# Kernel tuning notes

Measured on AMD Instinct MI355X. Metric: run time of the kernel, lower is better.

The kernel has to match this reference:

```python
import jax, jax.numpy as jnp
import numpy as np

N = 50000      # nodes
E = 800000     # top-down edges (before self-loops)
IN = 256       # in_dim
HID = 64       # hidden_dim
H = 4          # heads
SLOPE = 0.2    # PyG GATConv leaky_relu negative_slope


def setup_inputs() -> dict:
    key = jax.random.key(0)
    ks = jax.random.split(key, 12)
    g = lambda k, s, fan: jax.random.normal(k, s, dtype=jnp.float32) / np.float32(np.sqrt(fan))
    return {
        "x": jax.random.normal(ks[0], (N, IN), dtype=jnp.float32),
        "root_features": jax.random.normal(ks[1], (N, IN), dtype=jnp.float32),
        "edge_index": jax.random.randint(ks[2], (2, E), 0, N, dtype=jnp.int32),
        "W1": g(ks[3], (H * HID, IN), IN),
        "a_src1": g(ks[4], (H, HID), HID),
        "a_dst1": g(ks[5], (H, HID), HID),
        "b1": jnp.zeros((H * HID,), jnp.float32),
        "W2": g(ks[6], (H * HID, H * HID), H * HID),
        "a_src2": g(ks[7], (H, HID), HID),
        "a_dst2": g(ks[8], (H, HID), HID),
        "b2": jnp.zeros((HID,), jnp.float32),
        "Wr": g(ks[9], (HID, IN), IN),
        "br": jnp.zeros((HID,), jnp.float32),
    }


def gat_conv(h_in, src, dst, W, a_src, a_dst, bias, concat):
    """PyG GATConv (eval mode): gather -> attention logit -> segment softmax -> scatter."""
    h = (h_in @ W.T).reshape(-1, H, HID)                 # [N, H, C]
    alpha_s = jnp.einsum('nhc,hc->nh', h, a_src)         # [N, H]
    alpha_d = jnp.einsum('nhc,hc->nh', h, a_dst)
    logits = jax.nn.leaky_relu(alpha_s[src] + alpha_d[dst], SLOPE)   # [Etot, H]
    # numerically stable softmax over incoming edges of each dst node
    m = jax.ops.segment_max(logits, dst, num_segments=N)             # [N, H]
    e = jnp.exp(logits - m[dst])
    denom = jax.ops.segment_sum(e, dst, num_segments=N)              # [N, H]
    alpha = e / denom[dst]                                           # self-loops => denom > 0
    out = jax.ops.segment_sum(alpha[:, :, None] * h[src], dst, num_segments=N)  # [N, H, C]
    if concat:
        return out.reshape(-1, H * HID) + bias
    return out.mean(axis=1) + bias


def reference(x, root_features, edge_index, W1, a_src1, a_dst1, b1,
              W2, a_src2, a_dst2, b2, Wr, br):
    # PyG GATConv adds self-loops by default
    loops = jnp.arange(N, dtype=edge_index.dtype)
    src = jnp.concatenate([edge_index[0], loops])   # parents (message sources)
    dst = jnp.concatenate([edge_index[1], loops])   # children (aggregation targets)

    h = gat_conv(x, src, dst, W1, a_src1, a_dst1, b1, concat=True)   # [N, H*HID]
    h = jax.nn.relu(h)                                               # dropout = identity in eval
    h = gat_conv(h, src, dst, W2, a_src2, a_dst2, b2, concat=False)  # [N, HID]
    return h + root_features @ Wr.T + br
```

## Files before the change

kernel.cpp:

```cpp
#include <hip/hip_runtime.h>
#include <hip/hip_bf16.h>
#include <math.h>

#define NN   50000
#define EE   800000
#define ETOT (EE + NN)
#define KDIM 256
#define HEADS 4
#define HIDD 64
#define DCAP 64

typedef float  f32x4  __attribute__((ext_vector_type(4)));
typedef short  bf16x8 __attribute__((ext_vector_type(8)));

__device__ __forceinline__ float b2f(unsigned short u) {
    union { float f; unsigned int i; } v; v.i = (unsigned int)u << 16; return v.f;
}
__device__ __forceinline__ unsigned short f2b(float f) {
    union { float f; unsigned int i; } v; v.f = f;
    return (unsigned short)((v.i + 0x7fffu + ((v.i >> 16) & 1u)) >> 16);
}
__device__ __forceinline__ float lrelu(float x) { return x >= 0.f ? x : 0.2f * x; }

#define CASTB 144

__global__ __launch_bounds__(256) void prep_k(
    const float* __restrict__ W1, const float* __restrict__ W2,
    const float* __restrict__ Wr, unsigned short* __restrict__ wout)
{
    int i = (blockIdx.x * 256 + threadIdx.x) * 4;
    const float* src;
    int off;
    if (i < 65536)        { src = W1; off = 0; }
    else if (i < 131072)  { src = W2; off = 65536; }
    else                  { src = Wr; off = 131072; }
    float4 v = *reinterpret_cast<const float4*>(src + (i - off));
    ushort4 o;
    o.x = f2b(v.x); o.y = f2b(v.y); o.z = f2b(v.z); o.w = f2b(v.w);
    *reinterpret_cast<ushort4*>(wout + i) = o;
}

template<bool AF32, int NCT, bool ALPHA, bool OUTF32>
__device__ __forceinline__ void gemm_body(
    unsigned short* __restrict__ WlRaw, int bid,
    const void* __restrict__ Ain, const unsigned short* __restrict__ W,
    void* __restrict__ Cout, int Mrows,
    const float* __restrict__ av_src, const float* __restrict__ av_dst,
    float* __restrict__ AS, float* __restrict__ AD,
    const float* __restrict__ bias0, const float* __restrict__ bias1)
{
    constexpr int ROWS = NCT * 16;
    constexpr int KS   = 32;
    constexpr int LDK  = 40;
    constexpr int NSL  = KDIM / KS;
    constexpr int NLD  = (ROWS * KS) / (256 * 8);

    const int t    = threadIdx.x;
    const int wid  = t >> 6;
    const int lane = t & 63;
    const int cl   = lane & 15;
    const int kg   = lane >> 4;
    const int m0   = (bid * 4 + wid) * 16;

    int arow = m0 + cl; if (arow >= Mrows) arow = Mrows - 1;

    bf16x8 stg[NLD];
    auto LOADSTG = [&](int s) {
        #pragma unroll
        for (int i = 0; i < NLD; i++) {
            int f = i * 256 + t;
            int c = f >> 2, kc = f & 3;
            stg[i] = *reinterpret_cast<const bf16x8*>(
                W + (size_t)c * KDIM + s * KS + kc * 8);
        }
    };
    auto WRITESTG = [&](int b) {
        #pragma unroll
        for (int i = 0; i < NLD; i++) {
            int f = i * 256 + t;
            int c = f >> 2, kc = f & 3;
            *reinterpret_cast<bf16x8*>(&WlRaw[(size_t)(b * ROWS + c) * LDK + kc * 8]) = stg[i];
        }
    };
    auto LOADA = [&](int s) -> bf16x8 {
        if constexpr (AF32) {
            const float* ap = (const float*)Ain + (size_t)arow * KDIM + s * KS + kg * 8;
            float4 v0 = *reinterpret_cast<const float4*>(ap);
            float4 v1 = *reinterpret_cast<const float4*>(ap + 4);
            bf16x8 a;
            a[0] = (short)f2b(v0.x); a[1] = (short)f2b(v0.y);
            a[2] = (short)f2b(v0.z); a[3] = (short)f2b(v0.w);
            a[4] = (short)f2b(v1.x); a[5] = (short)f2b(v1.y);
            a[6] = (short)f2b(v1.z); a[7] = (short)f2b(v1.w);
            return a;
        } else {
            return *reinterpret_cast<const bf16x8*>(
                (const unsigned short*)Ain + (size_t)arow * KDIM + s * KS + kg * 8);
        }
    };

    f32x4 acc[NCT];
    #pragma unroll
    for (int ct = 0; ct < NCT; ct++) acc[ct] = (f32x4)(0.f);

    LOADSTG(0);
    WRITESTG(0);
    bf16x8 a_cur = LOADA(0);
    __syncthreads();

    int buf = 0;
    for (int s = 0; s < NSL; s++) {
        bf16x8 a_nxt;
        if (s + 1 < NSL) { LOADSTG(s + 1); a_nxt = LOADA(s + 1); }
        #pragma unroll
        for (int ct = 0; ct < NCT; ct++) {
            bf16x8 b = *reinterpret_cast<const bf16x8*>(
                &WlRaw[(size_t)(buf * ROWS + ct * 16 + cl) * LDK + kg * 8]);
            acc[ct] = __builtin_amdgcn_mfma_f32_16x16x32_bf16(a_cur, b, acc[ct], 0, 0, 0);
        }
        if (s + 1 < NSL) {
            WRITESTG(buf ^ 1);
            __syncthreads();
            buf ^= 1;
            a_cur = a_nxt;
        }
    }

    if constexpr (OUTF32) {
        float* C = (float*)Cout;
        #pragma unroll
        for (int ct = 0; ct < NCT; ct++) {
            #pragma unroll
            for (int r = 0; r < 4; r++) {
                int n = m0 + kg * 4 + r;
                int c = ct * 16 + cl;
                if (n < Mrows)
                    C[(size_t)n * (NCT * 16) + c] = acc[ct][r] + bias0[c] + bias1[c];
            }
        }
    } else {
        unsigned short* C = (unsigned short*)Cout;
        #pragma unroll
        for (int ct = 0; ct < NCT; ct++) {
            #pragma unroll
            for (int r = 0; r < 4; r++) {
                int n = m0 + kg * 4 + r;
                if (n < Mrows)
                    C[(size_t)n * (NCT * 16) + ct * 16 + cl] = f2b(acc[ct][r]);
            }
        }
    }

    if constexpr (ALPHA) {
        float asr[NCT], adr[NCT];
        #pragma unroll
        for (int ct = 0; ct < NCT; ct++) {
            int c = ct * 16 + cl;
            asr[ct] = av_src[c];
            adr[ct] = av_dst[c];
        }
        #pragma unroll
        for (int r = 0; r < 4; r++) {
            int n = m0 + kg * 4 + r;
            f32x4 s4 = (f32x4)(0.f), d4 = (f32x4)(0.f);
            #pragma unroll
            for (int h = 0; h < 4; h++) {
                #pragma unroll
                for (int q = 0; q < 4; q++) {
                    s4[h] += acc[h * 4 + q][r] * asr[h * 4 + q];
                    d4[h] += acc[h * 4 + q][r] * adr[h * 4 + q];
                }
            }
            #pragma unroll
            for (int msk = 1; msk <= 8; msk <<= 1) {
                #pragma unroll
                for (int h = 0; h < 4; h++) {
                    s4[h] += __shfl_xor(s4[h], msk, 64);
                    d4[h] += __shfl_xor(d4[h], msk, 64);
                }
            }
            if (cl == 0 && n < Mrows) {
                *reinterpret_cast<float4*>(AS + (size_t)n * 4) =
                    make_float4(s4[0], s4[1], s4[2], s4[3]);
                *reinterpret_cast<float4*>(AD + (size_t)n * 4) =
                    make_float4(d4[0], d4[1], d4[2], d4[3]);
            }
        }
    }
}

#define MG ((NN + 63) / 64)
#define EG ((ETOT + 255) / 256)

__global__ __launch_bounds__(256) void mega1_k(
    const float* __restrict__ x, const unsigned short* __restrict__ w1b,
    unsigned short* __restrict__ Hb,
    const float* __restrict__ as1, const float* __restrict__ ad1,
    float* __restrict__ AS, float* __restrict__ AD,
    const float* __restrict__ root, const unsigned short* __restrict__ wrb,
    float* __restrict__ out, const float* __restrict__ br, const float* __restrict__ b2,
    const int* __restrict__ ei, int* __restrict__ deg, int* __restrict__ EDG)
{
    __shared__ unsigned short Wl[2 * 256 * 40];
    int b = blockIdx.x;
    if (b < MG) {
        gemm_body<true, 16, true, false>(Wl, b, x, w1b, Hb, NN,
                                         as1, ad1, AS, AD, nullptr, nullptr);
    } else if (b < 2 * MG) {
        gemm_body<true, 4, false, true>(Wl, b - MG, root, wrb, out, NN,
                                        nullptr, nullptr, nullptr, nullptr, br, b2);
    } else {
        int e = (b - 2 * MG) * 256 + threadIdx.x;
        if (e < ETOT) {
            int src, dst;
            if (e < EE) { src = ei[e]; dst = ei[EE + e]; }
            else        { src = dst = e - EE; }
            int pos = atomicAdd(deg + dst, 1) & (DCAP - 1);
            EDG[(size_t)dst * DCAP + pos] = src;
        }
    }
}

__global__ __launch_bounds__(256) void gemm2_k(
    const unsigned short* __restrict__ X2b, const unsigned short* __restrict__ w2b,
    unsigned short* __restrict__ Hb,
    const float* __restrict__ as2, const float* __restrict__ ad2,
    float* __restrict__ AS, float* __restrict__ AD)
{
    __shared__ unsigned short Wl[2 * 256 * 40];
    gemm_body<false, 16, true, false>(Wl, blockIdx.x, X2b, w2b, Hb, NN,
                                      as2, ad2, AS, AD, nullptr, nullptr);
}

template<int MODE>
__global__ __launch_bounds__(256) void gather_k(
    const int* __restrict__ deg, const int* __restrict__ EDG,
    const float* __restrict__ AS, const float* __restrict__ AD,
    const unsigned short* __restrict__ H, const float* __restrict__ bias,
    unsigned short* __restrict__ OUT, float* __restrict__ OUTF)
{
    __shared__ float wT[4][4][65];
    int wid  = threadIdx.x >> 6;
    int lane = threadIdx.x & 63;
    int n = blockIdx.x * 4 + wid;
    if (n >= NN) return;
    int head = lane >> 4;

    int cd = min(deg[n], DCAP);
    float4 ad4 = *reinterpret_cast<const float4*>(AD + (size_t)n * 4);

    int srcv = (lane < cd) ? EDG[(size_t)n * DCAP + lane] : 0;
    float4 w4 = make_float4(0.f, 0.f, 0.f, 0.f);
    if (lane < cd) {
        float4 s4 = *reinterpret_cast<const float4*>(AS + (size_t)srcv * 4);
        w4.x = __expf(lrelu(s4.x + ad4.x));
        w4.y = __expf(lrelu(s4.y + ad4.y));
        w4.z = __expf(lrelu(s4.z + ad4.z));
        w4.w = __expf(lrelu(s4.w + ad4.w));
    }
    wT[wid][0][lane] = w4.x;
    wT[wid][1][lane] = w4.y;
    wT[wid][2][lane] = w4.z;
    wT[wid][3][lane] = w4.w;

    float4 den4 = w4;
    #pragma unroll
    for (int msk = 1; msk <= 32; msk <<= 1) {
        den4.x += __shfl_xor(den4.x, msk, 64);
        den4.y += __shfl_xor(den4.y, msk, 64);
        den4.z += __shfl_xor(den4.z, msk, 64);
        den4.w += __shfl_xor(den4.w, msk, 64);
    }
    float den = head == 0 ? den4.x : head == 1 ? den4.y : head == 2 ? den4.z : den4.w;
    float inv = 1.f / den;

    float a0 = 0.f, a1 = 0.f, a2 = 0.f, a3 = 0.f;
    float c0 = 0.f, c1 = 0.f, c2 = 0.f, c3 = 0.f;
    const unsigned short* hp = H + lane * 4;

    int j = 0;
    for (; j + 4 <= cd; j += 4) {
        int   sA = __builtin_amdgcn_readlane(srcv, j);
        int   sB = __builtin_amdgcn_readlane(srcv, j + 1);
        int   sC = __builtin_amdgcn_readlane(srcv, j + 2);
        int   sD = __builtin_amdgcn_readlane(srcv, j + 3);
        float wA = wT[wid][head][j];
        float wB = wT[wid][head][j + 1];
        float wC = wT[wid][head][j + 2];
        float wD = wT[wid][head][j + 3];
        ushort4 hA = *reinterpret_cast<const ushort4*>(hp + (size_t)sA * 256);
        ushort4 hB = *reinterpret_cast<const ushort4*>(hp + (size_t)sB * 256);
        ushort4 hC = *reinterpret_cast<const ushort4*>(hp + (size_t)sC * 256);
        ushort4 hD = *reinterpret_cast<const ushort4*>(hp + (size_t)sD * 256);
        a0 += wA * b2f(hA.x); a1 += wA * b2f(hA.y);
        a2 += wA * b2f(hA.z); a3 += wA * b2f(hA.w);
        c0 += wB * b2f(hB.x); c1 += wB * b2f(hB.y);
        c2 += wB * b2f(hB.z); c3 += wB * b2f(hB.w);
        a0 += wC * b2f(hC.x); a1 += wC * b2f(hC.y);
        a2 += wC * b2f(hC.z); a3 += wC * b2f(hC.w);
        c0 += wD * b2f(hD.x); c1 += wD * b2f(hD.y);
        c2 += wD * b2f(hD.z); c3 += wD * b2f(hD.w);
    }
    for (; j < cd; j++) {
        int   sA = __builtin_amdgcn_readlane(srcv, j);
        float wA = wT[wid][head][j];
        ushort4 hA = *reinterpret_cast<const ushort4*>(hp + (size_t)sA * 256);
        a0 += wA * b2f(hA.x); a1 += wA * b2f(hA.y);
        a2 += wA * b2f(hA.z); a3 += wA * b2f(hA.w);
    }
    a0 += c0; a1 += c1; a2 += c2; a3 += c3;

    if (MODE == 1) {
        float4 bv = *reinterpret_cast<const float4*>(bias + lane * 4);
        ushort4 o;
        o.x = f2b(fmaxf(a0 * inv + bv.x, 0.f));
        o.y = f2b(fmaxf(a1 * inv + bv.y, 0.f));
        o.z = f2b(fmaxf(a2 * inv + bv.z, 0.f));
        o.w = f2b(fmaxf(a3 * inv + bv.w, 0.f));
        *reinterpret_cast<ushort4*>(OUT + (size_t)n * 256 + lane * 4) = o;
    } else {
        float v0 = a0 * inv, v1 = a1 * inv, v2 = a2 * inv, v3 = a3 * inv;
        #pragma unroll
        for (int msk = 16; msk <= 32; msk <<= 1) {
            v0 += __shfl_xor(v0, msk, 64);
            v1 += __shfl_xor(v1, msk, 64);
            v2 += __shfl_xor(v2, msk, 64);
            v3 += __shfl_xor(v3, msk, 64);
        }
        if (lane < 16) {
            float4* o = reinterpret_cast<float4*>(OUTF + (size_t)n * 64 + lane * 4);
            float4 cur = *o;
            cur.x += 0.25f * v0;
            cur.y += 0.25f * v1;
            cur.z += 0.25f * v2;
            cur.w += 0.25f * v3;
            *o = cur;
        }
    }
}

extern "C" void kernel_launch(void* const* d_in, const int* in_sizes, int n_in,
                              void* d_out, int out_size, void* d_ws, size_t ws_size,
                              hipStream_t stream) {
    const float* x    = (const float*)d_in[0];
    const float* root = (const float*)d_in[1];
    const int*   ei   = (const int*)  d_in[2];
    const float* W1   = (const float*)d_in[3];
    const float* as1  = (const float*)d_in[4];
    const float* ad1  = (const float*)d_in[5];
    const float* b1   = (const float*)d_in[6];
    const float* W2   = (const float*)d_in[7];
    const float* as2  = (const float*)d_in[8];
    const float* ad2  = (const float*)d_in[9];
    const float* b2   = (const float*)d_in[10];
    const float* Wr   = (const float*)d_in[11];
    const float* br   = (const float*)d_in[12];
    float* out = (float*)d_out;

    unsigned short* Hb  = (unsigned short*)d_ws;
    unsigned short* X2b = Hb  + (size_t)NN * 256;
    unsigned short* w1b = X2b + (size_t)NN * 256;
    unsigned short* w2b = w1b + 65536;
    unsigned short* wrb = w2b + 65536;
    float* AS  = (float*)(wrb + 16384);
    float* AD  = AS + (size_t)NN * 4;
    int*   deg = (int*)(AD + (size_t)NN * 4);
    int*   EDG = deg + NN;

    const int wgrid = (NN + 3) / 4;

    hipMemsetAsync(deg, 0, NN * sizeof(int), stream);
    prep_k<<<CASTB, 256, 0, stream>>>(W1, W2, Wr, w1b);

    mega1_k<<<2 * MG + EG, 256, 0, stream>>>(x, w1b, Hb, as1, ad1, AS, AD,
                                             root, wrb, out, br, b2,
                                             ei, deg, EDG);
    gather_k<1><<<wgrid, 256, 0, stream>>>(deg, EDG, AS, AD, Hb, b1, X2b, nullptr);

    gemm2_k<<<MG, 256, 0, stream>>>(X2b, w2b, Hb, as2, ad2, AS, AD);
    gather_k<2><<<wgrid, 256, 0, stream>>>(deg, EDG, AS, AD, Hb, nullptr, nullptr, out);
}
```

Baseline: 257.9 us.

## Fold edge bucketing into a fifth wave of each GEMM block

```diff
diff --git a/kernel.cpp b/kernel.cpp
--- a/kernel.cpp
+++ b/kernel.cpp
@@ -42,7 +42,7 @@
 
 template<bool AF32, int NCT, bool ALPHA, bool OUTF32>
 __device__ __forceinline__ void gemm_body(
-    unsigned short* __restrict__ WlRaw, int bid,
+    unsigned short (*__restrict__ Wl)[40], int bid,
     const void* __restrict__ Ain, const unsigned short* __restrict__ W,
     void* __restrict__ Cout, int Mrows,
     const float* __restrict__ av_src, const float* __restrict__ av_dst,
@@ -51,7 +51,6 @@
 {
     constexpr int ROWS = NCT * 16;
     constexpr int KS   = 32;
-    constexpr int LDK  = 40;
     constexpr int NSL  = KDIM / KS;
     constexpr int NLD  = (ROWS * KS) / (256 * 8);
 
@@ -79,7 +78,7 @@
         for (int i = 0; i < NLD; i++) {
             int f = i * 256 + t;
             int c = f >> 2, kc = f & 3;
-            *reinterpret_cast<bf16x8*>(&WlRaw[(size_t)(b * ROWS + c) * LDK + kc * 8]) = stg[i];
+            *reinterpret_cast<bf16x8*>(&Wl[b * ROWS + c][kc * 8]) = stg[i];
         }
     };
     auto LOADA = [&](int s) -> bf16x8 {
@@ -114,8 +113,7 @@
         if (s + 1 < NSL) { LOADSTG(s + 1); a_nxt = LOADA(s + 1); }
         #pragma unroll
         for (int ct = 0; ct < NCT; ct++) {
-            bf16x8 b = *reinterpret_cast<const bf16x8*>(
-                &WlRaw[(size_t)(buf * ROWS + ct * 16 + cl) * LDK + kg * 8]);
+            bf16x8 b = *reinterpret_cast<const bf16x8*>(&Wl[buf * ROWS + ct * 16 + cl][kg * 8]);
             acc[ct] = __builtin_amdgcn_mfma_f32_16x16x32_bf16(a_cur, b, acc[ct], 0, 0, 0);
         }
         if (s + 1 < NSL) {
@@ -189,10 +187,10 @@
     }
 }
 
-#define MG ((NN + 63) / 64)
-#define EG ((ETOT + 255) / 256)
-
-__global__ __launch_bounds__(256) void mega1_k(
+#define MG   ((NN + 63) / 64)
+#define FCH  576
+
+__global__ __launch_bounds__(320) void mega1_k(
     const float* __restrict__ x, const unsigned short* __restrict__ w1b,
     unsigned short* __restrict__ Hb,
     const float* __restrict__ as1, const float* __restrict__ ad1,
@@ -201,22 +199,34 @@
     float* __restrict__ out, const float* __restrict__ br, const float* __restrict__ b2,
     const int* __restrict__ ei, int* __restrict__ deg, int* __restrict__ EDG)
 {
-    __shared__ unsigned short Wl[2 * 256 * 40];
-    int b = blockIdx.x;
-    if (b < MG) {
-        gemm_body<true, 16, true, false>(Wl, b, x, w1b, Hb, NN,
-                                         as1, ad1, AS, AD, nullptr, nullptr);
-    } else if (b < 2 * MG) {
-        gemm_body<true, 4, false, true>(Wl, b - MG, root, wrb, out, NN,
-                                        nullptr, nullptr, nullptr, nullptr, br, b2);
+    __shared__ unsigned short Wl[2 * 256][40];
+    const int b = blockIdx.x;
+    const int wid = threadIdx.x >> 6;
+
+    if (wid < 4) {
+        if (b < MG)
+            gemm_body<true, 16, true, false>(Wl, b, x, w1b, Hb, NN,
+                                             as1, ad1, AS, AD, nullptr, nullptr);
+        else
+            gemm_body<true, 4, false, true>(Wl, b - MG, root, wrb, out, NN,
+                                            nullptr, nullptr, nullptr, nullptr, br, b2);
     } else {
-        int e = (b - 2 * MG) * 256 + threadIdx.x;
-        if (e < ETOT) {
-            int src, dst;
-            if (e < EE) { src = ei[e]; dst = ei[EE + e]; }
-            else        { src = dst = e - EE; }
-            int pos = atomicAdd(deg + dst, 1) & (DCAP - 1);
-            EDG[(size_t)dst * DCAP + pos] = src;
+        const int lane = threadIdx.x & 63;
+        const int base = b * FCH;
+        auto doEdge = [&](int e) {
+            if (e < ETOT) {
+                int src, dst;
+                if (e < EE) { src = ei[e]; dst = ei[EE + e]; }
+                else        { src = dst = e - EE; }
+                int pos = atomicAdd(deg + dst, 1) & (DCAP - 1);
+                EDG[(size_t)dst * DCAP + pos] = src;
+            }
+        };
+        #pragma unroll
+        for (int s = 0; s < 8; s++) {
+            doEdge(base + s * 72 + lane);
+            if (lane < 8) doEdge(base + s * 72 + 64 + lane);
+            __syncthreads();
         }
     }
 }
@@ -227,7 +237,7 @@
     const float* __restrict__ as2, const float* __restrict__ ad2,
     float* __restrict__ AS, float* __restrict__ AD)
 {
-    __shared__ unsigned short Wl[2 * 256 * 40];
+    __shared__ unsigned short Wl[2 * 256][40];
     gemm_body<false, 16, true, false>(Wl, blockIdx.x, X2b, w2b, Hb, NN,
                                       as2, ad2, AS, AD, nullptr, nullptr);
 }
@@ -372,9 +382,9 @@
     hipMemsetAsync(deg, 0, NN * sizeof(int), stream);
     prep_k<<<CASTB, 256, 0, stream>>>(W1, W2, Wr, w1b);
 
-    mega1_k<<<2 * MG + EG, 256, 0, stream>>>(x, w1b, Hb, as1, ad1, AS, AD,
-                                             root, wrb, out, br, b2,
-                                             ei, deg, EDG);
+    mega1_k<<<2 * MG, 320, 0, stream>>>(x, w1b, Hb, as1, ad1, AS, AD,
+                                        root, wrb, out, br, b2,
+                                        ei, deg, EDG);
     gather_k<1><<<wgrid, 256, 0, stream>>>(deg, EDG, AS, AD, Hb, b1, X2b, nullptr);
 
     gemm2_k<<<MG, 256, 0, stream>>>(X2b, w2b, Hb, as2, ad2, AS, AD);
```

Result: faster. 237.2 us (median of 2 runs) (-8.0%).
